# Kernel optimization log

Hardware: AMD Instinct MI355X
Metric: run time of the kernel (lower is better)

The kernel has to match this reference:

```python
import jax, jax.numpy as jnp
import numpy as np

B, C, H, W = 8, 512, 96, 96
CQ = 64  # inter_ch


def setup_inputs() -> dict:
    key = jax.random.key(0)
    ks = jax.random.split(key, 8)
    scale = 1.0 / np.sqrt(C)
    return {
        "x": jax.random.normal(ks[0], (B, C, H, W), dtype=jnp.float32),
        "Wq": jax.random.normal(ks[1], (CQ, C), dtype=jnp.float32) * scale,
        "bq": jax.random.normal(ks[2], (CQ,), dtype=jnp.float32) * 0.01,
        "Wk": jax.random.normal(ks[3], (CQ, C), dtype=jnp.float32) * scale,
        "bk": jax.random.normal(ks[4], (CQ,), dtype=jnp.float32) * 0.01,
        "Wv": jax.random.normal(ks[5], (C, C), dtype=jnp.float32) * scale,
        "bv": jax.random.normal(ks[6], (C,), dtype=jnp.float32) * 0.01,
        "gamma": jax.random.normal(ks[7], (1,), dtype=jnp.float32) * 0.1,
    }


def reference(x, Wq, bq, Wk, bk, Wv, bv, gamma):
    # 1x1 convs expressed as channel matmuls; outputs in BHWC layout
    Q = jnp.einsum('bchw,oc->bhwo', x, Wq) + bq   # [B,H,W,CQ]
    K = jnp.einsum('bchw,oc->bhwo', x, Wk) + bk   # [B,H,W,CQ]
    V = jnp.einsum('bchw,oc->bhwo', x, Wv) + bv   # [B,H,W,C]

    # Per pixel (i,j): keys = concat(row i keys [W], column j keys [H]).
    # NOTE: this replication includes pixel (i,j) twice (once in row, once in col),
    # matching the torch loop exactly (no -INF masking as in original CCNet).
    e_row = jnp.einsum('bhwc,bhvc->bhwv', Q, K)   # [B,H,W,W] attend along row h
    e_col = jnp.einsum('bhwc,bgwc->bhwg', Q, K)   # [B,H,W,H] attend along col w
    attn = jax.nn.softmax(jnp.concatenate([e_row, e_col], axis=-1), axis=-1)
    a_row, a_col = attn[..., :W], attn[..., W:]   # [B,H,W,W], [B,H,W,H]

    out = (jnp.einsum('bhwv,bhvc->bhwc', a_row, V)
           + jnp.einsum('bhwg,bgwc->bhwc', a_col, V))  # [B,H,W,C]
    out = jnp.transpose(out, (0, 3, 1, 2))        # [B,C,H,W]
    return x + gamma[0] * out
```

## Files before the change

kernel.cpp:

```cpp
#include <hip/hip_runtime.h>
#include <stdint.h>

#define B_  8
#define C_  512
#define H_  96
#define W_  96
#define CQ_ 64
#define P_  (H_*W_)
#define NP  (B_*P_)
#define L_  (W_+H_)

typedef __attribute__((ext_vector_type(8))) short short8;
typedef __attribute__((ext_vector_type(4))) float f32x4;

__device__ __forceinline__ ushort f2bf(float f) {
    uint32_t u = __builtin_bit_cast(uint32_t, f);
    u += 0x7fff + ((u >> 16) & 1);
    return (ushort)(u >> 16);
}
__device__ __forceinline__ float bf2f(ushort h) {
    uint32_t u = ((uint32_t)h) << 16;
    return __builtin_bit_cast(float, u);
}

__global__ __launch_bounds__(256) void k_xt(const float* __restrict__ x, ushort* __restrict__ xt) {
    __shared__ float tile[64][65];
    int p0 = blockIdx.x * 64, c0 = blockIdx.y * 64, bat = blockIdx.z;
    int tx = threadIdx.x, ty = threadIdx.y;
    const float* xb = x + ((size_t)bat * C_ + c0) * P_ + p0;
    #pragma unroll
    for (int i = ty; i < 64; i += 8) {
        float2 v = *(const float2*)&xb[(size_t)i * P_ + 2 * tx];
        tile[i][2 * tx] = v.x; tile[i][2 * tx + 1] = v.y;
    }
    __syncthreads();
    ushort* o = xt + ((size_t)bat * P_ + p0) * C_ + c0;
    #pragma unroll
    for (int i = ty; i < 64; i += 8) {
        ushort2 v; v.x = f2bf(tile[2 * tx][i]); v.y = f2bf(tile[2 * tx + 1][i]);
        *(ushort2*)&o[(size_t)i * C_ + 2 * tx] = v;
    }
}

__global__ __launch_bounds__(256) void k_wconv(const float* __restrict__ Wq, const float* __restrict__ Wk,
                                               const float* __restrict__ Wv, const float* __restrict__ bq,
                                               const float* __restrict__ bk, const float* __restrict__ bv,
                                               ushort* __restrict__ Wall, float* __restrict__ ball) {
    int idx = blockIdx.x * 256 + threadIdx.x;
    if (idx < 640) {
        float b;
        if (idx < 64)       b = bq[idx];
        else if (idx < 128) b = bk[idx - 64];
        else                b = bv[idx - 128];
        ball[idx] = b;
    }
    if (idx >= 640 * C_) return;
    int o = idx / C_, c = idx % C_;
    float v;
    if (o < 64)       v = Wq[o * C_ + c];
    else if (o < 128) v = Wk[(o - 64) * C_ + c];
    else              v = Wv[(o - 128) * C_ + c];
    Wall[idx] = f2bf(v);
}

#define LSTR 40
__global__ __launch_bounds__(512) void k_qkv(const ushort* __restrict__ xt, const ushort* __restrict__ Wall,
                                             const float* __restrict__ ball,
                                             ushort* __restrict__ Qcm, ushort* __restrict__ Kcm,
                                             ushort* __restrict__ Vcm) {
    __shared__ __align__(16) ushort Al[640 * LSTR];
    __shared__ __align__(16) ushort Bl[128 * LSTR];
    int tid = threadIdx.x, lane = tid & 63, wvid = tid >> 6;
    int wrm = wvid >> 1, wcn = wvid & 1;
    int r0 = blockIdx.x * 128;
    f32x4 acc[10][4] = {};
    for (int kb = 0; kb < C_; kb += 32) {
        #pragma unroll
        for (int s = 0; s < 5; ++s) {
            int idx = tid + s * 512, row = idx >> 2, seg = idx & 3;
            *(short8*)&Al[row * LSTR + seg * 8] = *(const short8*)&Wall[(size_t)row * C_ + kb + seg * 8];
        }
        {
            int row = tid >> 2, seg = tid & 3;
            *(short8*)&Bl[row * LSTR + seg * 8] = *(const short8*)&xt[(size_t)(r0 + row) * C_ + kb + seg * 8];
        }
        __syncthreads();
        int rr = lane & 15, gq = lane >> 4;
        short8 fb[4];
        #pragma unroll
        for (int nt = 0; nt < 4; ++nt) fb[nt] = *(const short8*)&Bl[(wcn * 64 + nt * 16 + rr) * LSTR + gq * 8];
        #pragma unroll
        for (int mt = 0; mt < 10; ++mt) {
            short8 fa = *(const short8*)&Al[(wrm * 160 + mt * 16 + rr) * LSTR + gq * 8];
            #pragma unroll
            for (int nt = 0; nt < 4; ++nt)
                acc[mt][nt] = __builtin_amdgcn_mfma_f32_16x16x32_bf16(fa, fb[nt], acc[mt][nt], 0, 0, 0);
        }
        __syncthreads();
    }
    int rr = lane & 15, gq = lane >> 4;
    int bat = r0 / P_, pb = r0 % P_;
    #pragma unroll
    for (int mt = 0; mt < 10; ++mt)
        #pragma unroll
        for (int nt = 0; nt < 4; ++nt) {
            int col = wcn * 64 + nt * 16 + rr;
            #pragma unroll
            for (int q = 0; q < 4; ++q) {
                int o = wrm * 160 + mt * 16 + gq * 4 + q;
                float v = acc[mt][nt][q] + ball[o];
                if (o < 64)       Qcm[(size_t)o * NP + r0 + col] = f2bf(v);
                else if (o < 128) Kcm[(size_t)(o - 64) * NP + r0 + col] = f2bf(v);
                else              Vcm[((size_t)bat * C_ + (o - 128)) * P_ + pb + col] = f2bf(v);
            }
        }
}

__global__ __launch_bounds__(256) void k_qkt(const ushort* __restrict__ Qcm, const ushort* __restrict__ Kcm,
                                             ushort* __restrict__ Qb, ushort* __restrict__ Kb) {
    __shared__ ushort t[64][65];
    int p0 = blockIdx.x * 64;
    const ushort* src = blockIdx.y ? Kcm : Qcm;
    ushort* dst = blockIdx.y ? Kb : Qb;
    int tx = threadIdx.x, ty = threadIdx.y;
    #pragma unroll
    for (int i = ty; i < 64; i += 4) t[i][tx] = src[(size_t)i * NP + p0 + tx];
    __syncthreads();
    #pragma unroll
    for (int i = ty; i < 64; i += 4) dst[(size_t)(p0 + i) * CQ_ + tx] = t[tx][i];
}

__global__ __launch_bounds__(256) void k_vt(const ushort* __restrict__ Vcm, ushort* __restrict__ Vt) {
    __shared__ ushort t[32][33];
    int tile = blockIdx.x; int h0 = (tile / 3) * 32, w0 = (tile % 3) * 32;
    int c = blockIdx.y, bat = blockIdx.z;
    int tx = threadIdx.x, ty = threadIdx.y;
    const ushort* src = Vcm + ((size_t)(bat * C_ + c)) * P_;
    #pragma unroll
    for (int i = ty; i < 32; i += 8) t[i][tx] = src[(h0 + i) * W_ + w0 + tx];
    __syncthreads();
    #pragma unroll
    for (int i = ty; i < 32; i += 8)
        Vt[((size_t)(bat * W_ + w0 + i) * C_ + c) * H_ + h0 + tx] = t[tx][i];
}

__global__ __launch_bounds__(256) void k_erow(const ushort* __restrict__ Qb, const ushort* __restrict__ Kb,
                                              float* __restrict__ logits) {
    __shared__ __align__(16) ushort Al[96 * LSTR];
    __shared__ __align__(16) ushort Bl[96 * LSTR];
    int h = blockIdx.x, bat = blockIdx.y;
    int tid = threadIdx.x, lane = tid & 63, wvid = tid >> 6;
    int wr = wvid >> 1, wc = wvid & 1;
    size_t base = ((size_t)bat * H_ + h) * W_;
    f32x4 acc[3][3] = {};
    for (int kb = 0; kb < CQ_; kb += 32) {
        for (int s = tid; s < 96 * 4; s += 256) {
            int row = s >> 2, seg = s & 3;
            *(short8*)&Al[row * LSTR + seg * 8] = *(const short8*)&Qb[(base + row) * CQ_ + kb + seg * 8];
            *(short8*)&Bl[row * LSTR + seg * 8] = *(const short8*)&Kb[(base + row) * CQ_ + kb + seg * 8];
        }
        __syncthreads();
        int rr = lane & 15, gq = lane >> 4;
        #pragma unroll
        for (int mt = 0; mt < 3; ++mt) {
            short8 fa = *(const short8*)&Al[(wr * 48 + mt * 16 + rr) * LSTR + gq * 8];
            #pragma unroll
            for (int nt = 0; nt < 3; ++nt) {
                short8 fb = *(const short8*)&Bl[(wc * 48 + nt * 16 + rr) * LSTR + gq * 8];
                acc[mt][nt] = __builtin_amdgcn_mfma_f32_16x16x32_bf16(fa, fb, acc[mt][nt], 0, 0, 0);
            }
        }
        __syncthreads();
    }
    int rr = lane & 15, gq = lane >> 4;
    #pragma unroll
    for (int mt = 0; mt < 3; ++mt)
        #pragma unroll
        for (int nt = 0; nt < 3; ++nt)
            #pragma unroll
            for (int q = 0; q < 4; ++q) {
                int w = wr * 48 + mt * 16 + gq * 4 + q;
                int v = wc * 48 + nt * 16 + rr;
                logits[(base + w) * L_ + v] = acc[mt][nt][q];
            }
}

__global__ __launch_bounds__(256) void k_ecol(const ushort* __restrict__ Qb, const ushort* __restrict__ Kb,
                                              float* __restrict__ logits) {
    __shared__ __align__(16) ushort Al[96 * LSTR];
    __shared__ __align__(16) ushort Bl[96 * LSTR];
    int w = blockIdx.x, bat = blockIdx.y;
    int tid = threadIdx.x, lane = tid & 63, wvid = tid >> 6;
    int wr = wvid >> 1, wc = wvid & 1;
    f32x4 acc[3][3] = {};
    for (int kb = 0; kb < CQ_; kb += 32) {
        for (int s = tid; s < 96 * 4; s += 256) {
            int row = s >> 2, seg = s & 3;
            size_t px = ((size_t)bat * H_ + row) * W_ + w;
            *(short8*)&Al[row * LSTR + seg * 8] = *(const short8*)&Qb[px * CQ_ + kb + seg * 8];
            *(short8*)&Bl[row * LSTR + seg * 8] = *(const short8*)&Kb[px * CQ_ + kb + seg * 8];
        }
        __syncthreads();
        int rr = lane & 15, gq = lane >> 4;
        #pragma unroll
        for (int mt = 0; mt < 3; ++mt) {
            short8 fa = *(const short8*)&Al[(wr * 48 + mt * 16 + rr) * LSTR + gq * 8];
            #pragma unroll
            for (int nt = 0; nt < 3; ++nt) {
                short8 fb = *(const short8*)&Bl[(wc * 48 + nt * 16 + rr) * LSTR + gq * 8];
                acc[mt][nt] = __builtin_amdgcn_mfma_f32_16x16x32_bf16(fa, fb, acc[mt][nt], 0, 0, 0);
            }
        }
        __syncthreads();
    }
    int rr = lane & 15, gq = lane >> 4;
    #pragma unroll
    for (int mt = 0; mt < 3; ++mt)
        #pragma unroll
        for (int nt = 0; nt < 3; ++nt)
            #pragma unroll
            for (int q = 0; q < 4; ++q) {
                int hh = wr * 48 + mt * 16 + gq * 4 + q;
                int gg = wc * 48 + nt * 16 + rr;
                logits[(((size_t)bat * H_ + hh) * W_ + w) * L_ + W_ + gg] = acc[mt][nt][q];
            }
}

__global__ __launch_bounds__(256) void k_softmax(const float* __restrict__ logits, ushort* __restrict__ attn) {
    int wvid = threadIdx.x >> 6, lane = threadIdx.x & 63;
    size_t px = (size_t)blockIdx.x * 4 + wvid;
    const float* lp = logits + px * L_;
    float v0 = lp[lane], v1 = lp[lane + 64], v2 = lp[lane + 128];
    float m = fmaxf(fmaxf(v0, v1), v2);
    #pragma unroll
    for (int off = 32; off; off >>= 1) m = fmaxf(m, __shfl_xor(m, off));
    float e0 = __expf(v0 - m), e1 = __expf(v1 - m), e2 = __expf(v2 - m);
    float s = e0 + e1 + e2;
    #pragma unroll
    for (int off = 32; off; off >>= 1) s += __shfl_xor(s, off);
    float inv = 1.0f / s;
    ushort* ap = attn + px * L_;
    ap[lane] = f2bf(e0 * inv); ap[lane + 64] = f2bf(e1 * inv); ap[lane + 128] = f2bf(e2 * inv);
}

__global__ __launch_bounds__(512) void k_pvrow(const ushort* __restrict__ Vcm, const ushort* __restrict__ attn,
                                               ushort* __restrict__ out0) {
    __shared__ __align__(16) ushort Al[512 * LSTR];
    __shared__ __align__(16) ushort Bl[96 * LSTR];
    int h = blockIdx.x, bat = blockIdx.y;
    int tid = threadIdx.x, lane = tid & 63, wvid = tid >> 6;
    int wrm = wvid >> 1, wcn = wvid & 1;
    size_t vbase = (size_t)bat * C_ * P_ + (size_t)h * W_;
    size_t abase = ((size_t)bat * H_ + h) * W_ * L_;
    f32x4 acc[8][3] = {};
    for (int kb = 0; kb < 96; kb += 32) {
        #pragma unroll
        for (int s = 0; s < 4; ++s) {
            int idx = tid + s * 512, row = idx >> 2, seg = idx & 3;
            *(short8*)&Al[row * LSTR + seg * 8] = *(const short8*)&Vcm[vbase + (size_t)row * P_ + kb + seg * 8];
        }
        if (tid < 384) {
            int row = tid >> 2, seg = tid & 3;
            *(short8*)&Bl[row * LSTR + seg * 8] = *(const short8*)&attn[abase + (size_t)row * L_ + kb + seg * 8];
        }
        __syncthreads();
        int rr = lane & 15, gq = lane >> 4;
        short8 fb[3];
        #pragma unroll
        for (int nt = 0; nt < 3; ++nt) fb[nt] = *(const short8*)&Bl[(wcn * 48 + nt * 16 + rr) * LSTR + gq * 8];
        #pragma unroll
        for (int mt = 0; mt < 8; ++mt) {
            short8 fa = *(const short8*)&Al[(wrm * 128 + mt * 16 + rr) * LSTR + gq * 8];
            #pragma unroll
            for (int nt = 0; nt < 3; ++nt)
                acc[mt][nt] = __builtin_amdgcn_mfma_f32_16x16x32_bf16(fa, fb[nt], acc[mt][nt], 0, 0, 0);
        }
        __syncthreads();
    }
    int rr = lane & 15, gq = lane >> 4;
    #pragma unroll
    for (int mt = 0; mt < 8; ++mt)
        #pragma unroll
        for (int nt = 0; nt < 3; ++nt) {
            int w = wcn * 48 + nt * 16 + rr;
            #pragma unroll
            for (int q = 0; q < 4; ++q) {
                int c = wrm * 128 + mt * 16 + gq * 4 + q;
                out0[((size_t)bat * C_ + c) * P_ + (size_t)h * W_ + w] = f2bf(acc[mt][nt][q]);
            }
        }
}

__global__ __launch_bounds__(512) void k_pvcol(const ushort* __restrict__ Vt, const ushort* __restrict__ attn,
                                               ushort* __restrict__ out1t) {
    __shared__ __align__(16) ushort Al[512 * LSTR];
    __shared__ __align__(16) ushort Bl[96 * LSTR];
    int w = blockIdx.x, bat = blockIdx.y;
    int tid = threadIdx.x, lane = tid & 63, wvid = tid >> 6;
    int wrm = wvid >> 1, wcn = wvid & 1;
    size_t vbase = ((size_t)bat * W_ + w) * C_ * H_;
    size_t abase = ((size_t)bat * P_ + w) * L_ + W_;
    f32x4 acc[8][3] = {};
    for (int kb = 0; kb < 96; kb += 32) {
        #pragma unroll
        for (int s = 0; s < 4; ++s) {
            int idx = tid + s * 512, row = idx >> 2, seg = idx & 3;
            *(short8*)&Al[row * LSTR + seg * 8] = *(const short8*)&Vt[vbase + (size_t)row * H_ + kb + seg * 8];
        }
        if (tid < 384) {
            int row = tid >> 2, seg = tid & 3;
            *(short8*)&Bl[row * LSTR + seg * 8] = *(const short8*)&attn[abase + (size_t)row * (W_ * L_) + kb + seg * 8];
        }
        __syncthreads();
        int rr = lane & 15, gq = lane >> 4;
        short8 fb[3];
        #pragma unroll
        for (int nt = 0; nt < 3; ++nt) fb[nt] = *(const short8*)&Bl[(wcn * 48 + nt * 16 + rr) * LSTR + gq * 8];
        #pragma unroll
        for (int mt = 0; mt < 8; ++mt) {
            short8 fa = *(const short8*)&Al[(wrm * 128 + mt * 16 + rr) * LSTR + gq * 8];
            #pragma unroll
            for (int nt = 0; nt < 3; ++nt)
                acc[mt][nt] = __builtin_amdgcn_mfma_f32_16x16x32_bf16(fa, fb[nt], acc[mt][nt], 0, 0, 0);
        }
        __syncthreads();
    }
    int rr = lane & 15, gq = lane >> 4;
    #pragma unroll
    for (int mt = 0; mt < 8; ++mt)
        #pragma unroll
        for (int nt = 0; nt < 3; ++nt) {
            int hh = wcn * 48 + nt * 16 + rr;
            #pragma unroll
            for (int q = 0; q < 4; ++q) {
                int c = wrm * 128 + mt * 16 + gq * 4 + q;
                out1t[((size_t)(bat * C_ + c) * W_ + w) * H_ + hh] = f2bf(acc[mt][nt][q]);
            }
        }
}

__global__ __launch_bounds__(256) void k_final(const float* __restrict__ x, const ushort* __restrict__ out0,
                                               const ushort* __restrict__ out1t, const float* __restrict__ gamma,
                                               float* __restrict__ out) {
    __shared__ ushort t[96 * 98];
    int c = blockIdx.x, bat = blockIdx.y;
    const ushort* src = out1t + ((size_t)bat * C_ + c) * P_;
    int tid = threadIdx.x;
    for (int i = tid; i < 4608; i += 256) {
        int w = i / 48, h = (i % 48) * 2;
        ushort2 v = *(const ushort2*)&src[w * 96 + h];
        *(ushort2*)&t[w * 98 + h] = v;
    }
    __syncthreads();
    float gm = gamma[0];
    size_t base = ((size_t)bat * C_ + c) * P_;
    for (int i = tid; i < 4608; i += 256) {
        int h = i / 48, w = (i % 48) * 2;
        size_t idx = base + h * W_ + w;
        float2 xv = *(const float2*)&x[idx];
        ushort2 o0 = *(const ushort2*)&out0[idx];
        float2 r;
        r.x = xv.x + gm * (bf2f(o0.x) + bf2f(t[w * 98 + h]));
        r.y = xv.y + gm * (bf2f(o0.y) + bf2f(t[(w + 1) * 98 + h]));
        *(float2*)&out[idx] = r;
    }
}

extern "C" void kernel_launch(void* const* d_in, const int* in_sizes, int n_in,
                              void* d_out, int out_size, void* d_ws, size_t ws_size,
                              hipStream_t stream) {
    const float* x     = (const float*)d_in[0];
    const float* Wq    = (const float*)d_in[1];
    const float* bq    = (const float*)d_in[2];
    const float* Wk    = (const float*)d_in[3];
    const float* bk    = (const float*)d_in[4];
    const float* Wv    = (const float*)d_in[5];
    const float* bv    = (const float*)d_in[6];
    const float* gamma = (const float*)d_in[7];
    float* out = (float*)d_out;
    char* ws = (char*)d_ws;

    const size_t SZ  = (size_t)NP * C_ * 2;
    const size_t QKS = (size_t)NP * CQ_ * 2;
    ushort* Qcm    = (ushort*)(ws);
    ushort* Kcm    = (ushort*)(ws + QKS);
    float*  logits = (float*) (ws + 2 * QKS);
    ushort* out1t  = (ushort*)(ws);
    ushort* xt     = (ushort*)(ws + SZ);
    ushort* out0   = xt;
    ushort* Vcm    = (ushort*)(ws + 2 * SZ);
    ushort* Vt     = (ushort*)(ws + 3 * SZ);
    ushort* Qb     = (ushort*)(ws + 4 * SZ);
    ushort* Kb     = (ushort*)(ws + 4 * SZ + QKS);
    ushort* attn   = (ushort*)(ws + 4 * SZ);
    ushort* Wall   = (ushort*)(ws + 4 * SZ + (size_t)NP * L_ * 2);
    float*  ball   = (float*) (ws + 4 * SZ + (size_t)NP * L_ * 2 + 640 * C_ * 2);

    k_xt     <<<dim3(144, 8, 8),  dim3(32, 8), 0, stream>>>(x, xt);
    k_wconv  <<<dim3(1280),       dim3(256),   0, stream>>>(Wq, Wk, Wv, bq, bk, bv, Wall, ball);
    k_qkv    <<<dim3(576),        dim3(512),   0, stream>>>(xt, Wall, ball, Qcm, Kcm, Vcm);
    k_qkt    <<<dim3(1152, 2),    dim3(64, 4), 0, stream>>>(Qcm, Kcm, Qb, Kb);
    k_vt     <<<dim3(9, 512, 8),  dim3(32, 8), 0, stream>>>(Vcm, Vt);
    k_erow   <<<dim3(96, 8),      dim3(256),   0, stream>>>(Qb, Kb, logits);
    k_ecol   <<<dim3(96, 8),      dim3(256),   0, stream>>>(Qb, Kb, logits);
    k_softmax<<<dim3(NP / 4),     dim3(256),   0, stream>>>(logits, attn);
    k_pvrow  <<<dim3(96, 8),      dim3(512),   0, stream>>>(Vcm, attn, out0);
    k_pvcol  <<<dim3(96, 8),      dim3(512),   0, stream>>>(Vt, attn, out1t);
    k_final  <<<dim3(512, 8),     dim3(256),   0, stream>>>(x, out0, out1t, gamma, out);
}
```

Before: 428.7 us.

## Retile QKV projection with direct-to-LDS loads, rework V transpose, bf16 residual copy

```diff
diff --git a/kernel.cpp b/kernel.cpp
--- a/kernel.cpp
+++ b/kernel.cpp
@@ -12,6 +12,7 @@
 
 typedef __attribute__((ext_vector_type(8))) short short8;
 typedef __attribute__((ext_vector_type(4))) float f32x4;
+typedef __attribute__((ext_vector_type(4))) unsigned short us4;
 
 __device__ __forceinline__ ushort f2bf(float f) {
     uint32_t u = __builtin_bit_cast(uint32_t, f);
@@ -23,7 +24,12 @@
     return __builtin_bit_cast(float, u);
 }
 
-__global__ __launch_bounds__(256) void k_xt(const float* __restrict__ x, ushort* __restrict__ xt) {
+#define GLL16(g, l) __builtin_amdgcn_global_load_lds( \
+    (const __attribute__((address_space(1))) uint32_t*)(g), \
+    (__attribute__((address_space(3))) uint32_t*)(l), 16, 0, 0)
+
+__global__ __launch_bounds__(256) void k_xt(const float* __restrict__ x, ushort* __restrict__ xt,
+                                            ushort* __restrict__ xbc, int use_xbc) {
     __shared__ float tile[64][65];
     int p0 = blockIdx.x * 64, c0 = blockIdx.y * 64, bat = blockIdx.z;
     int tx = threadIdx.x, ty = threadIdx.y;
@@ -32,6 +38,10 @@
     for (int i = ty; i < 64; i += 8) {
         float2 v = *(const float2*)&xb[(size_t)i * P_ + 2 * tx];
         tile[i][2 * tx] = v.x; tile[i][2 * tx + 1] = v.y;
+        if (use_xbc) {
+            ushort2 bv; bv.x = f2bf(v.x); bv.y = f2bf(v.y);
+            *(ushort2*)&xbc[((size_t)bat * C_ + c0 + i) * P_ + p0 + 2 * tx] = bv;
+        }
     }
     __syncthreads();
     ushort* o = xt + ((size_t)bat * P_ + p0) * C_ + c0;
@@ -63,35 +73,33 @@
     Wall[idx] = f2bf(v);
 }
 
-#define LSTR 40
-__global__ __launch_bounds__(512) void k_qkv(const ushort* __restrict__ xt, const ushort* __restrict__ Wall,
-                                             const float* __restrict__ ball,
-                                             ushort* __restrict__ Qcm, ushort* __restrict__ Kcm,
-                                             ushort* __restrict__ Vcm) {
-    __shared__ __align__(16) ushort Al[640 * LSTR];
-    __shared__ __align__(16) ushort Bl[128 * LSTR];
-    int tid = threadIdx.x, lane = tid & 63, wvid = tid >> 6;
-    int wrm = wvid >> 1, wcn = wvid & 1;
-    int r0 = blockIdx.x * 128;
-    f32x4 acc[10][4] = {};
+__global__ __launch_bounds__(256, 4) void k_proj(const ushort* __restrict__ xt, const ushort* __restrict__ Wall,
+                                                 const float* __restrict__ ball,
+                                                 ushort* __restrict__ Qcm, ushort* __restrict__ Kcm,
+                                                 ushort* __restrict__ Vcm) {
+    __shared__ __align__(16) ushort Al[128 * 32];
+    __shared__ __align__(16) ushort Bl[128 * 32];
+    int tid = threadIdx.x, lane = tid & 63, wv = tid >> 6;
+    int wr = wv >> 1, wc = wv & 1;
+    int wg = ((int)blockIdx.x & 7) * 360 + ((int)blockIdx.x >> 3);
+    int m0 = (wg % 5) * 128;
+    int n0 = (wg / 5) * 128;
+    f32x4 acc[4][4] = {};
     for (int kb = 0; kb < C_; kb += 32) {
         #pragma unroll
-        for (int s = 0; s < 5; ++s) {
-            int idx = tid + s * 512, row = idx >> 2, seg = idx & 3;
-            *(short8*)&Al[row * LSTR + seg * 8] = *(const short8*)&Wall[(size_t)row * C_ + kb + seg * 8];
-        }
-        {
-            int row = tid >> 2, seg = tid & 3;
-            *(short8*)&Bl[row * LSTR + seg * 8] = *(const short8*)&xt[(size_t)(r0 + row) * C_ + kb + seg * 8];
+        for (int i = 0; i < 2; ++i) {
+            int u = tid + i * 256, row = u >> 2, seg = u & 3;
+            GLL16(&Wall[(size_t)(m0 + row) * C_ + kb + seg * 8], &Al[(size_t)u * 8]);
+            GLL16(&xt[(size_t)(n0 + row) * C_ + kb + seg * 8],   &Bl[(size_t)u * 8]);
         }
         __syncthreads();
         int rr = lane & 15, gq = lane >> 4;
         short8 fb[4];
         #pragma unroll
-        for (int nt = 0; nt < 4; ++nt) fb[nt] = *(const short8*)&Bl[(wcn * 64 + nt * 16 + rr) * LSTR + gq * 8];
-        #pragma unroll
-        for (int mt = 0; mt < 10; ++mt) {
-            short8 fa = *(const short8*)&Al[(wrm * 160 + mt * 16 + rr) * LSTR + gq * 8];
+        for (int nt = 0; nt < 4; ++nt) fb[nt] = *(const short8*)&Bl[(wc * 64 + nt * 16 + rr) * 32 + gq * 8];
+        #pragma unroll
+        for (int mt = 0; mt < 4; ++mt) {
+            short8 fa = *(const short8*)&Al[(wr * 64 + mt * 16 + rr) * 32 + gq * 8];
             #pragma unroll
             for (int nt = 0; nt < 4; ++nt)
                 acc[mt][nt] = __builtin_amdgcn_mfma_f32_16x16x32_bf16(fa, fb[nt], acc[mt][nt], 0, 0, 0);
@@ -99,19 +107,19 @@
         __syncthreads();
     }
     int rr = lane & 15, gq = lane >> 4;
-    int bat = r0 / P_, pb = r0 % P_;
-    #pragma unroll
-    for (int mt = 0; mt < 10; ++mt)
+    int bat = n0 / P_, pb0 = n0 - bat * P_;
+    #pragma unroll
+    for (int mt = 0; mt < 4; ++mt)
         #pragma unroll
         for (int nt = 0; nt < 4; ++nt) {
-            int col = wcn * 64 + nt * 16 + rr;
+            int col = wc * 64 + nt * 16 + rr;
             #pragma unroll
             for (int q = 0; q < 4; ++q) {
-                int o = wrm * 160 + mt * 16 + gq * 4 + q;
+                int o = m0 + wr * 64 + mt * 16 + gq * 4 + q;
                 float v = acc[mt][nt][q] + ball[o];
-                if (o < 64)       Qcm[(size_t)o * NP + r0 + col] = f2bf(v);
-                else if (o < 128) Kcm[(size_t)(o - 64) * NP + r0 + col] = f2bf(v);
-                else              Vcm[((size_t)bat * C_ + (o - 128)) * P_ + pb + col] = f2bf(v);
+                if (o < 64)       Qcm[(size_t)o * NP + n0 + col] = f2bf(v);
+                else if (o < 128) Kcm[(size_t)(o - 64) * NP + n0 + col] = f2bf(v);
+                else              Vcm[((size_t)bat * C_ + (o - 128)) * P_ + pb0 + col] = f2bf(v);
             }
         }
 }
@@ -131,19 +139,31 @@
 }
 
 __global__ __launch_bounds__(256) void k_vt(const ushort* __restrict__ Vcm, ushort* __restrict__ Vt) {
-    __shared__ ushort t[32][33];
-    int tile = blockIdx.x; int h0 = (tile / 3) * 32, w0 = (tile % 3) * 32;
-    int c = blockIdx.y, bat = blockIdx.z;
-    int tx = threadIdx.x, ty = threadIdx.y;
+    __shared__ ushort t[96 * 98];
+    int c = blockIdx.x, bat = blockIdx.y;
     const ushort* src = Vcm + ((size_t)(bat * C_ + c)) * P_;
-    #pragma unroll
-    for (int i = ty; i < 32; i += 8) t[i][tx] = src[(h0 + i) * W_ + w0 + tx];
+    int tid = threadIdx.x;
+    for (int u = tid; u < 2304; u += 256) {
+        int h = u / 24, w4 = (u % 24) * 4;
+        us4 v = *(const us4*)&src[h * 96 + w4];
+        ushort2 a; a.x = v.x; a.y = v.y;
+        ushort2 b; b.x = v.z; b.y = v.w;
+        *(ushort2*)&t[h * 98 + w4]     = a;
+        *(ushort2*)&t[h * 98 + w4 + 2] = b;
+    }
     __syncthreads();
-    #pragma unroll
-    for (int i = ty; i < 32; i += 8)
-        Vt[((size_t)(bat * W_ + w0 + i) * C_ + c) * H_ + h0 + tx] = t[tx][i];
-}
-
+    for (int u = tid; u < 2304; u += 256) {
+        int w = u / 24, h4 = (u % 24) * 4;
+        us4 o;
+        o.x = t[(h4 + 0) * 98 + w];
+        o.y = t[(h4 + 1) * 98 + w];
+        o.z = t[(h4 + 2) * 98 + w];
+        o.w = t[(h4 + 3) * 98 + w];
+        *(us4*)&Vt[((size_t)(bat * W_ + w) * C_ + c) * H_ + h4] = o;
+    }
+}
+
+#define LSTR 40
 __global__ __launch_bounds__(256) void k_erow(const ushort* __restrict__ Qb, const ushort* __restrict__ Kb,
                                               float* __restrict__ logits) {
     __shared__ __align__(16) ushort Al[96 * LSTR];
@@ -243,10 +263,10 @@
     ap[lane] = f2bf(e0 * inv); ap[lane + 64] = f2bf(e1 * inv); ap[lane + 128] = f2bf(e2 * inv);
 }
 
-__global__ __launch_bounds__(512) void k_pvrow(const ushort* __restrict__ Vcm, const ushort* __restrict__ attn,
-                                               ushort* __restrict__ out0) {
-    __shared__ __align__(16) ushort Al[512 * LSTR];
-    __shared__ __align__(16) ushort Bl[96 * LSTR];
+__global__ __launch_bounds__(512, 4) void k_pvrow(const ushort* __restrict__ Vcm, const ushort* __restrict__ attn,
+                                                  ushort* __restrict__ out0) {
+    __shared__ __align__(16) ushort Al[512 * 32];
+    __shared__ __align__(16) ushort Bl[96 * 32];
     int h = blockIdx.x, bat = blockIdx.y;
     int tid = threadIdx.x, lane = tid & 63, wvid = tid >> 6;
     int wrm = wvid >> 1, wcn = wvid & 1;
@@ -255,22 +275,22 @@
     f32x4 acc[8][3] = {};
     for (int kb = 0; kb < 96; kb += 32) {
         #pragma unroll
-        for (int s = 0; s < 4; ++s) {
-            int idx = tid + s * 512, row = idx >> 2, seg = idx & 3;
-            *(short8*)&Al[row * LSTR + seg * 8] = *(const short8*)&Vcm[vbase + (size_t)row * P_ + kb + seg * 8];
+        for (int i = 0; i < 4; ++i) {
+            int u = tid + i * 512, row = u >> 2, seg = u & 3;
+            GLL16(&Vcm[vbase + (size_t)row * P_ + kb + seg * 8], &Al[(size_t)u * 8]);
         }
         if (tid < 384) {
             int row = tid >> 2, seg = tid & 3;
-            *(short8*)&Bl[row * LSTR + seg * 8] = *(const short8*)&attn[abase + (size_t)row * L_ + kb + seg * 8];
+            GLL16(&attn[abase + (size_t)row * L_ + kb + seg * 8], &Bl[(size_t)tid * 8]);
         }
         __syncthreads();
         int rr = lane & 15, gq = lane >> 4;
         short8 fb[3];
         #pragma unroll
-        for (int nt = 0; nt < 3; ++nt) fb[nt] = *(const short8*)&Bl[(wcn * 48 + nt * 16 + rr) * LSTR + gq * 8];
+        for (int nt = 0; nt < 3; ++nt) fb[nt] = *(const short8*)&Bl[(wcn * 48 + nt * 16 + rr) * 32 + gq * 8];
         #pragma unroll
         for (int mt = 0; mt < 8; ++mt) {
-            short8 fa = *(const short8*)&Al[(wrm * 128 + mt * 16 + rr) * LSTR + gq * 8];
+            short8 fa = *(const short8*)&Al[(wrm * 128 + mt * 16 + rr) * 32 + gq * 8];
             #pragma unroll
             for (int nt = 0; nt < 3; ++nt)
                 acc[mt][nt] = __builtin_amdgcn_mfma_f32_16x16x32_bf16(fa, fb[nt], acc[mt][nt], 0, 0, 0);
@@ -291,10 +311,10 @@
         }
 }
 
-__global__ __launch_bounds__(512) void k_pvcol(const ushort* __restrict__ Vt, const ushort* __restrict__ attn,
-                                               ushort* __restrict__ out1t) {
-    __shared__ __align__(16) ushort Al[512 * LSTR];
-    __shared__ __align__(16) ushort Bl[96 * LSTR];
+__global__ __launch_bounds__(512, 4) void k_pvcol(const ushort* __restrict__ Vt, const ushort* __restrict__ attn,
+                                                  ushort* __restrict__ out1t) {
+    __shared__ __align__(16) ushort Al[512 * 32];
+    __shared__ __align__(16) ushort Bl[96 * 32];
     int w = blockIdx.x, bat = blockIdx.y;
     int tid = threadIdx.x, lane = tid & 63, wvid = tid >> 6;
     int wrm = wvid >> 1, wcn = wvid & 1;
@@ -303,22 +323,22 @@
     f32x4 acc[8][3] = {};
     for (int kb = 0; kb < 96; kb += 32) {
         #pragma unroll
-        for (int s = 0; s < 4; ++s) {
-            int idx = tid + s * 512, row = idx >> 2, seg = idx & 3;
-            *(short8*)&Al[row * LSTR + seg * 8] = *(const short8*)&Vt[vbase + (size_t)row * H_ + kb + seg * 8];
+        for (int i = 0; i < 4; ++i) {
+            int u = tid + i * 512, row = u >> 2, seg = u & 3;
+            GLL16(&Vt[vbase + (size_t)row * H_ + kb + seg * 8], &Al[(size_t)u * 8]);
         }
         if (tid < 384) {
             int row = tid >> 2, seg = tid & 3;
-            *(short8*)&Bl[row * LSTR + seg * 8] = *(const short8*)&attn[abase + (size_t)row * (W_ * L_) + kb + seg * 8];
+            GLL16(&attn[abase + (size_t)row * (W_ * L_) + kb + seg * 8], &Bl[(size_t)tid * 8]);
         }
         __syncthreads();
         int rr = lane & 15, gq = lane >> 4;
         short8 fb[3];
         #pragma unroll
-        for (int nt = 0; nt < 3; ++nt) fb[nt] = *(const short8*)&Bl[(wcn * 48 + nt * 16 + rr) * LSTR + gq * 8];
+        for (int nt = 0; nt < 3; ++nt) fb[nt] = *(const short8*)&Bl[(wcn * 48 + nt * 16 + rr) * 32 + gq * 8];
         #pragma unroll
         for (int mt = 0; mt < 8; ++mt) {
-            short8 fa = *(const short8*)&Al[(wrm * 128 + mt * 16 + rr) * LSTR + gq * 8];
+            short8 fa = *(const short8*)&Al[(wrm * 128 + mt * 16 + rr) * 32 + gq * 8];
             #pragma unroll
             for (int nt = 0; nt < 3; ++nt)
                 acc[mt][nt] = __builtin_amdgcn_mfma_f32_16x16x32_bf16(fa, fb[nt], acc[mt][nt], 0, 0, 0);
@@ -339,9 +359,10 @@
         }
 }
 
-__global__ __launch_bounds__(256) void k_final(const float* __restrict__ x, const ushort* __restrict__ out0,
-                                               const ushort* __restrict__ out1t, const float* __restrict__ gamma,
-                                               float* __restrict__ out) {
+__global__ __launch_bounds__(256) void k_final(const float* __restrict__ x, const ushort* __restrict__ xbc,
+                                               const ushort* __restrict__ out0, const ushort* __restrict__ out1t,
+                                               const float* __restrict__ gamma, float* __restrict__ out,
+                                               int use_xbc) {
     __shared__ ushort t[96 * 98];
     int c = blockIdx.x, bat = blockIdx.y;
     const ushort* src = out1t + ((size_t)bat * C_ + c) * P_;
@@ -357,11 +378,18 @@
     for (int i = tid; i < 4608; i += 256) {
         int h = i / 48, w = (i % 48) * 2;
         size_t idx = base + h * W_ + w;
-        float2 xv = *(const float2*)&x[idx];
+        float xa, xbv;
+        if (use_xbc) {
+            ushort2 xv = *(const ushort2*)&xbc[idx];
+            xa = bf2f(xv.x); xbv = bf2f(xv.y);
+        } else {
+            float2 xv = *(const float2*)&x[idx];
+            xa = xv.x; xbv = xv.y;
+        }
         ushort2 o0 = *(const ushort2*)&out0[idx];
         float2 r;
-        r.x = xv.x + gm * (bf2f(o0.x) + bf2f(t[w * 98 + h]));
-        r.y = xv.y + gm * (bf2f(o0.y) + bf2f(t[(w + 1) * 98 + h]));
+        r.x = xa  + gm * (bf2f(o0.x) + bf2f(t[w * 98 + h]));
+        r.y = xbv + gm * (bf2f(o0.y) + bf2f(t[(w + 1) * 98 + h]));
         *(float2*)&out[idx] = r;
     }
 }
@@ -393,18 +421,22 @@
     ushort* Qb     = (ushort*)(ws + 4 * SZ);
     ushort* Kb     = (ushort*)(ws + 4 * SZ + QKS);
     ushort* attn   = (ushort*)(ws + 4 * SZ);
-    ushort* Wall   = (ushort*)(ws + 4 * SZ + (size_t)NP * L_ * 2);
-    float*  ball   = (float*) (ws + 4 * SZ + (size_t)NP * L_ * 2 + 640 * C_ * 2);
-
-    k_xt     <<<dim3(144, 8, 8),  dim3(32, 8), 0, stream>>>(x, xt);
+    size_t off_wall = 4 * SZ + (size_t)NP * L_ * 2;
+    ushort* Wall   = (ushort*)(ws + off_wall);
+    float*  ball   = (float*) (ws + off_wall + 640 * C_ * 2);
+    size_t off_xbc = off_wall + 640 * C_ * 2 + 4096;
+    ushort* xbc    = (ushort*)(ws + off_xbc);
+    int use_xbc = (ws_size >= off_xbc + SZ) ? 1 : 0;
+
+    k_xt     <<<dim3(144, 8, 8),  dim3(32, 8), 0, stream>>>(x, xt, xbc, use_xbc);
     k_wconv  <<<dim3(1280),       dim3(256),   0, stream>>>(Wq, Wk, Wv, bq, bk, bv, Wall, ball);
-    k_qkv    <<<dim3(576),        dim3(512),   0, stream>>>(xt, Wall, ball, Qcm, Kcm, Vcm);
+    k_proj   <<<dim3(2880),       dim3(256),   0, stream>>>(xt, Wall, ball, Qcm, Kcm, Vcm);
     k_qkt    <<<dim3(1152, 2),    dim3(64, 4), 0, stream>>>(Qcm, Kcm, Qb, Kb);
-    k_vt     <<<dim3(9, 512, 8),  dim3(32, 8), 0, stream>>>(Vcm, Vt);
+    k_vt     <<<dim3(512, 8),     dim3(256),   0, stream>>>(Vcm, Vt);
     k_erow   <<<dim3(96, 8),      dim3(256),   0, stream>>>(Qb, Kb, logits);
     k_ecol   <<<dim3(96, 8),      dim3(256),   0, stream>>>(Qb, Kb, logits);
     k_softmax<<<dim3(NP / 4),     dim3(256),   0, stream>>>(logits, attn);
     k_pvrow  <<<dim3(96, 8),      dim3(512),   0, stream>>>(Vcm, attn, out0);
     k_pvcol  <<<dim3(96, 8),      dim3(512),   0, stream>>>(Vt, attn, out1t);
-    k_final  <<<dim3(512, 8),     dim3(256),   0, stream>>>(x, out0, out1t, gamma, out);
-}
+    k_final  <<<dim3(512, 8),     dim3(256),   0, stream>>>(x, xbc, out0, out1t, gamma, out, use_xbc);
+}
```

New measurement: 461.1 us. 1.08x slower.
